# Kernel tuning notes

Hardware: AMD Instinct MI355X
Metric: run time of the kernel (lower is better)

## Reference

```python
import jax, jax.numpy as jnp
import numpy as np

B, C, T = 8, 128, 32768
OUT, K, DIL = 128, 2, 2


def dilated_indices(T, k, d):
    # Faithful vectorized version of the original Python double loop:
    # idx[span*k + j] = span + j*d, clamped to T (the zero-pad slot) when >= T+1.
    padded = T + 1
    idx = jnp.arange(padded)[:, None] + jnp.arange(k)[None, :] * d  # (padded, k)
    idx = idx.reshape(-1)                                           # (k*padded,)
    return jnp.where(idx >= padded, T, idx)


def setup_inputs() -> dict:
    key = jax.random.key(0)
    k1, k2, k3 = jax.random.split(key, 3)
    x = jax.random.normal(k1, (B, C, T), dtype=jnp.float32)
    # Conv1d(in=C, out=OUT, kernel_size=K) parameters
    W = jax.random.normal(k2, (OUT, C, K), dtype=jnp.float32) * 0.05
    b = jax.random.normal(k3, (OUT,), dtype=jnp.float32) * 0.05
    return {"x": x, "W": W, "b": b}


def reference(x, W, b):
    Bx, Cx, Tx = x.shape
    # pad one zero column at the end of the time axis (torch.cat with zeros)
    xp = jnp.concatenate([x, jnp.zeros((Bx, Cx, 1), x.dtype)], axis=2)  # (B,C,T+1)
    idx = dilated_indices(Tx, K, DIL)                                   # (K*(T+1),)
    swizzle = xp[:, :, idx]                                             # (B,C,K*(T+1))
    # Conv1d with stride == kernel_size over the swizzled buffer is a GEMM
    # over non-overlapping windows of size K.
    sw = swizzle.reshape(Bx, Cx, Tx + 1, K)                             # (B,C,T+1,K)
    out = jnp.einsum('bcpk,ock->bop', sw, W) + b[None, :, None]         # (B,OUT,T+1)
    return out
```

## Files before the change

### kernel.cpp

```cpp
#include <hip/hip_runtime.h>


namespace {

constexpr int kB   = 8;
constexpr int kC   = 128;
constexpr int kT   = 32768;
constexpr int kP   = kT + 1;
constexpr int kOut = 128;
constexpr int kNP  = 128;
constexpr int kNTiles = (kP + kNP - 1) / kNP;
constexpr int kLStride = 136;

typedef __attribute__((ext_vector_type(8))) short short8;
typedef __attribute__((ext_vector_type(4))) float f32x4;

__device__ __forceinline__ short f2bf(float f) {
    unsigned int u = __builtin_bit_cast(unsigned int, f);
    u += 0x7fffu + ((u >> 16) & 1u);
    return (short)(u >> 16);
}

template <bool GUARD>
__device__ __forceinline__ void stage_tile(const float* __restrict__ xb,
                                           short* __restrict__ xs,
                                           int tid, int p0) {
    {
        const int pos = tid & 127;
        const int gp  = p0 + pos;
        const bool ok = !GUARD || (gp < kT);
        const float* col = xb + (ok ? gp : 0);
        const int c0base = (tid >> 7) * 64;
        #pragma unroll
        for (int ch = 0; ch < 8; ++ch) {
            const int c0 = c0base + ch * 8;
            float r[8];
            #pragma unroll
            for (int j = 0; j < 8; ++j) r[j] = col[(c0 + j) << 15];
            short8 v;
            #pragma unroll
            for (int j = 0; j < 8; ++j) v[j] = ok ? f2bf(r[j]) : (short)0;
            *reinterpret_cast<short8*>(xs + pos * kLStride + c0) = v;
        }
    }
    if (tid < 32) {
        const int pos = 128 + (tid & 1);
        const int gp  = p0 + pos;
        const bool ok = !GUARD || (gp < kT);
        const float* col = xb + (ok ? gp : 0);
        const int c0 = (tid >> 1) * 8;
        float r[8];
        #pragma unroll
        for (int j = 0; j < 8; ++j) r[j] = col[(c0 + j) << 15];
        short8 v;
        #pragma unroll
        for (int j = 0; j < 8; ++j) v[j] = ok ? f2bf(r[j]) : (short)0;
        *reinterpret_cast<short8*>(xs + pos * kLStride + c0) = v;
    }
}

__global__ __launch_bounds__(256, 2) void dconv_mfma(
    const float* __restrict__ x, const float* __restrict__ W,
    const float* __restrict__ bias, float* __restrict__ out)
{
    __shared__ __align__(16) short xs[130 * kLStride];

    const int tid  = threadIdx.x;
    const int lane = tid & 63;
    const int wv   = tid >> 6;
    const int bb   = blockIdx.x / kNTiles;
    const int tile = blockIdx.x % kNTiles;
    const int p0   = tile * kNP;

    const int rowbase = wv * 32;
    short8 wf[2][2][4];
    #pragma unroll
    for (int cc = 0; cc < 2; ++cc) {
        const int o = rowbase + cc * 16 + (lane & 15);
        #pragma unroll
        for (int s = 0; s < 4; ++s) {
            const int cb = s * 32 + (lane >> 4) * 8;
            const float4* wp = reinterpret_cast<const float4*>(W + o * (kC * 2) + cb * 2);
            float4 wr[4];
            #pragma unroll
            for (int q = 0; q < 4; ++q) wr[q] = wp[q];
            short8 f0, f1;
            #pragma unroll
            for (int q = 0; q < 4; ++q) {
                f0[q * 2 + 0] = f2bf(wr[q].x);  f1[q * 2 + 0] = f2bf(wr[q].y);
                f0[q * 2 + 1] = f2bf(wr[q].z);  f1[q * 2 + 1] = f2bf(wr[q].w);
            }
            wf[0][cc][s] = f0;
            wf[1][cc][s] = f1;
        }
    }

    const float* xb = x + (size_t)bb * kC * kT;
    if (p0 + 129 < kT) stage_tile<false>(xb, xs, tid, p0);
    else               stage_tile<true>(xb, xs, tid, p0);

    f32x4 acc[2][8];
    #pragma unroll
    for (int cc = 0; cc < 2; ++cc) {
        const int ob = rowbase + cc * 16 + (lane >> 4) * 4;
        f32x4 a;
        a[0] = bias[ob + 0]; a[1] = bias[ob + 1];
        a[2] = bias[ob + 2]; a[3] = bias[ob + 3];
        #pragma unroll
        for (int nc = 0; nc < 8; ++nc) acc[cc][nc] = a;
    }

    __syncthreads();

    #pragma unroll
    for (int tap = 0; tap < 2; ++tap) {
        #pragma unroll
        for (int s = 0; s < 4; ++s) {
            const int cb = s * 32 + (lane >> 4) * 8;
            #pragma unroll
            for (int nc = 0; nc < 8; ++nc) {
                const int pos = nc * 16 + (lane & 15) + 2 * tap;
                const short8 bf = *reinterpret_cast<const short8*>(xs + pos * kLStride + cb);
                acc[0][nc] = __builtin_amdgcn_mfma_f32_16x16x32_bf16(wf[tap][0][s], bf, acc[0][nc], 0, 0, 0);
                acc[1][nc] = __builtin_amdgcn_mfma_f32_16x16x32_bf16(wf[tap][1][s], bf, acc[1][nc], 0, 0, 0);
            }
        }
    }

    float* ob = out + (size_t)bb * kOut * kP;
    #pragma unroll
    for (int nc = 0; nc < 8; ++nc) {
        const int col = p0 + nc * 16 + (lane & 15);
        if (col < kP) {
            #pragma unroll
            for (int cc = 0; cc < 2; ++cc) {
                const int orow = rowbase + cc * 16 + (lane >> 4) * 4;
                #pragma unroll
                for (int r = 0; r < 4; ++r) {
                    ob[(size_t)(orow + r) * kP + col] = acc[cc][nc][r];
                }
            }
        }
    }
}

}

extern "C" void kernel_launch(void* const* d_in, const int* in_sizes, int n_in,
                              void* d_out, int out_size, void* d_ws, size_t ws_size,
                              hipStream_t stream) {
    const float* x    = (const float*)d_in[0];
    const float* W    = (const float*)d_in[1];
    const float* bias = (const float*)d_in[2];
    float* out        = (float*)d_out;

    dim3 grid(kB * kNTiles);
    dim3 block(256);
    hipLaunchKernelGGL(dconv_mfma, grid, block, 0, stream, x, W, bias, out);
}
```

Baseline: 281.6 us.

## Vectorize input staging with float4 loads and transpose into LDS

Replaces per-element strided scalar global loads in the tile staging with float4 loads along the time axis, where each thread loads 16 channels × 4 positions and transposes them in registers into the channel-contiguous LDS layout. The halo columns are loaded with one scalar per thread. Launch bounds are raised to 3 blocks per CU to allow more occupancy. The 16 float4 registers per thread raise register pressure, which may conflict with the higher occupancy target, and the LDS stores may hit bank conflicts.

```diff
diff --git a/kernel.cpp b/kernel.cpp
--- a/kernel.cpp
+++ b/kernel.cpp
@@ -21,45 +21,61 @@
     return (short)(u >> 16);
 }
 
-template <bool GUARD>
-__device__ __forceinline__ void stage_tile(const float* __restrict__ xb,
+__device__ __forceinline__ void stage_fast(const float* __restrict__ xb,
                                            short* __restrict__ xs,
                                            int tid, int p0) {
-    {
-        const int pos = tid & 127;
-        const int gp  = p0 + pos;
-        const bool ok = !GUARD || (gp < kT);
-        const float* col = xb + (ok ? gp : 0);
-        const int c0base = (tid >> 7) * 64;
+    const int g     = tid >> 5;
+    const int chunk = tid & 31;
+    const float* base = xb + p0 + chunk * 4;
+    float4 r[16];
+    #pragma unroll
+    for (int i = 0; i < 16; ++i)
+        r[i] = *reinterpret_cast<const float4*>(base + (size_t)(g * 16 + i) * kT);
+
+    const int hc = tid & 127, hp = 128 + (tid >> 7);
+    const float hv = xb[(size_t)hc * kT + p0 + hp];
+
+    #pragma unroll
+    for (int j = 0; j < 4; ++j) {
+        short8 s0, s1;
         #pragma unroll
-        for (int ch = 0; ch < 8; ++ch) {
-            const int c0 = c0base + ch * 8;
-            float r[8];
-            #pragma unroll
-            for (int j = 0; j < 8; ++j) r[j] = col[(c0 + j) << 15];
-            short8 v;
-            #pragma unroll
-            for (int j = 0; j < 8; ++j) v[j] = ok ? f2bf(r[j]) : (short)0;
-            *reinterpret_cast<short8*>(xs + pos * kLStride + c0) = v;
+        for (int i = 0; i < 8; ++i) {
+            s0[i] = f2bf(reinterpret_cast<const float*>(&r[i])[j]);
+            s1[i] = f2bf(reinterpret_cast<const float*>(&r[i + 8])[j]);
         }
+        short* row = xs + (chunk * 4 + j) * kLStride + g * 16;
+        *reinterpret_cast<short8*>(row)     = s0;
+        *reinterpret_cast<short8*>(row + 8) = s1;
     }
-    if (tid < 32) {
-        const int pos = 128 + (tid & 1);
-        const int gp  = p0 + pos;
-        const bool ok = !GUARD || (gp < kT);
-        const float* col = xb + (ok ? gp : 0);
-        const int c0 = (tid >> 1) * 8;
-        float r[8];
-        #pragma unroll
-        for (int j = 0; j < 8; ++j) r[j] = col[(c0 + j) << 15];
-        short8 v;
-        #pragma unroll
-        for (int j = 0; j < 8; ++j) v[j] = ok ? f2bf(r[j]) : (short)0;
-        *reinterpret_cast<short8*>(xs + pos * kLStride + c0) = v;
-    }
+    xs[hp * kLStride + hc] = f2bf(hv);
 }
 
-__global__ __launch_bounds__(256, 2) void dconv_mfma(
+__device__ __forceinline__ void stage_guard(const float* __restrict__ xb,
+                                            short* __restrict__ xs,
+                                            int tid, int p0) {
+    const int g     = tid >> 5;
+    const int chunk = tid & 31;
+    #pragma unroll
+    for (int j = 0; j < 4; ++j) {
+        const int gp = p0 + chunk * 4 + j;
+        const bool ok = gp < kT;
+        short8 s0, s1;
+        #pragma unroll
+        for (int i = 0; i < 8; ++i) {
+            const int c0 = g * 16 + i;
+            s0[i] = ok ? f2bf(xb[(size_t)c0 * kT + gp]) : (short)0;
+            s1[i] = ok ? f2bf(xb[(size_t)(c0 + 8) * kT + gp]) : (short)0;
+        }
+        short* row = xs + (chunk * 4 + j) * kLStride + g * 16;
+        *reinterpret_cast<short8*>(row)     = s0;
+        *reinterpret_cast<short8*>(row + 8) = s1;
+    }
+    const int hc = tid & 127, hp = 128 + (tid >> 7);
+    const int gp = p0 + hp;
+    xs[hp * kLStride + hc] = (gp < kT) ? f2bf(xb[(size_t)hc * kT + gp]) : (short)0;
+}
+
+__global__ __launch_bounds__(256, 3) void dconv_mfma(
     const float* __restrict__ x, const float* __restrict__ W,
     const float* __restrict__ bias, float* __restrict__ out)
 {
@@ -96,8 +112,8 @@
     }
 
     const float* xb = x + (size_t)bb * kC * kT;
-    if (p0 + 129 < kT) stage_tile<false>(xb, xs, tid, p0);
-    else               stage_tile<true>(xb, xs, tid, p0);
+    if (p0 + 129 < kT) stage_fast(xb, xs, tid, p0);
+    else               stage_guard(xb, xs, tid, p0);
 
     f32x4 acc[2][8];
     #pragma unroll
```

New measurement: 320.8 us. 1.14x slower.
